# Performance work log

Measured on AMD Instinct MI355X. Metric: run time of the kernel, lower is better.

Reference implementation:

```python
import jax, jax.numpy as jnp
import numpy as np

EPS = 1e-4


def setup_inputs() -> dict:
    key = jax.random.key(0)
    k1, k2, k3, k4, k5 = jax.random.split(key, 5)
    N, M, F = 2048, 2048, 128
    embeds = jax.random.uniform(k1, (N, F), dtype=jnp.float32)
    base_embeds = jax.random.normal(k2, (M, F), dtype=jnp.float32)
    base_rewards = jax.random.normal(k3, (M,), dtype=jnp.float32)
    # torch Linear(num_feat, num_feat, bias=False) / Linear(num_feat, 1, bias=False)
    # stored here as [in, out] for x @ W convention
    W1 = jax.random.normal(k4, (F, F), dtype=jnp.float32) / np.sqrt(F)
    w2 = jax.random.normal(k5, (F, 1), dtype=jnp.float32) / np.sqrt(F)
    return {"embeds": embeds, "base_embeds": base_embeds,
            "base_rewards": base_rewards, "W1": W1, "w2": w2}


def reference(embeds, base_embeds, base_rewards, W1, w2):
    # pairwise differences: [N, M, F]
    diff = embeds[:, None, :] - base_embeds[None, :, :]
    # tiny MLP distance kernel: Linear -> ELU -> Linear, abs
    h = jax.nn.elu(jnp.einsum('nmf,fg->nmg', diff, W1))
    dist = jnp.abs(jnp.einsum('nmg,go->nmo', h, w2)[:, :, 0])  # [N, M]
    # inverse-distance normalized weights
    dist_w = 1.0 / (dist + EPS)
    dist_w = dist_w / jnp.sum(dist_w, axis=1, keepdims=True)
    rewards = jnp.sum(dist_w * base_rewards[None, :], axis=1)  # [N]
    return rewards
```

## Files before the change

kernel.cpp:

```cpp
#include <hip/hip_runtime.h>
#include <hip/hip_bf16.h>

#define F      128
#define NROWS  2048
#define MROWS  2048
#define BN     128
#define BM     64
#define MT     (MROWS/BM)
#define GC     32
#define NCH    (F/GC)
#define LDS_W  36
#define LOG2E  1.44269504088896340736f

typedef float f32x2 __attribute__((ext_vector_type(2)));
typedef float f32x4 __attribute__((ext_vector_type(4)));

__device__ __forceinline__ f32x2 lo2(f32x4 v) { return __builtin_shufflevector(v, v, 0, 1); }
__device__ __forceinline__ f32x2 hi2(f32x4 v) { return __builtin_shufflevector(v, v, 2, 3); }

__global__ __launch_bounds__(256) void proj_kernel(
    const float* __restrict__ embeds, const float* __restrict__ base,
    const float* __restrict__ W1, const float* __restrict__ w2,
    float* __restrict__ A1, float* __restrict__ AE,
    float* __restrict__ B1, float* __restrict__ BE,
    float* __restrict__ w2sum)
{
    const int tid = threadIdx.x;
    const int sub = tid >> 7;
    const int g   = tid & 127;
    const int row = blockIdx.x * 2 + sub;

    __shared__ float xs[2][F];
    {
        const float* src = (row < NROWS) ? &embeds[(size_t)row * F]
                                         : &base[(size_t)(row - NROWS) * F];
        xs[sub][g] = src[g];
    }
    __syncthreads();

    float acc = 0.0f;
#pragma unroll 8
    for (int f = 0; f < F; ++f)
        acc = fmaf(xs[sub][f], W1[f * F + g], acc);

    if (row < NROWS) {
        const size_t idx = (size_t)row * F + g;
        A1[idx] = acc + 1.0f;
        AE[idx] = __builtin_amdgcn_exp2f(acc * LOG2E);
    } else {
        const size_t idx = (size_t)(row - NROWS) * F + g;
        B1[idx] = -acc;
        BE[idx] = __builtin_amdgcn_exp2f(-acc * LOG2E);
    }

    if (blockIdx.x == 0 && tid < 64) {
        float s = w2[tid] + w2[tid + 64];
#pragma unroll
        for (int k = 1; k < 64; k <<= 1) s += __shfl_xor(s, k);
        if (tid == 0) *w2sum = s;
    }
}

__global__ __launch_bounds__(256) void pair_kernel(
    const float* __restrict__ A1, const float* __restrict__ AE,
    const float* __restrict__ B1, const float* __restrict__ BE,
    const float* __restrict__ w2, const float* __restrict__ w2sum_p,
    const float* __restrict__ brew, float* __restrict__ partials)
{
    __shared__ float As1[BN][LDS_W], AsE[BN][LDS_W];
    __shared__ float Bs1[BM][LDS_W], BsE[BM][LDS_W];
    __shared__ float w2s[F];
    __shared__ float rs[BM];

    const int tid = threadIdx.x;
    const int nt  = blockIdx.x;
    const int mt  = blockIdx.y;
    const int tr  = tid >> 4;
    const int tc  = tid & 15;

    f32x2 acc2[8][4];
#pragma unroll
    for (int i = 0; i < 8; ++i)
#pragma unroll
        for (int j = 0; j < 4; ++j) acc2[i][j] = (f32x2)(0.0f);

    if (tid < F)                 w2s[tid]     = w2[tid];
    else if (tid < F + BM)       rs[tid - F]  = brew[mt * BM + (tid - F)];

#pragma unroll 1
    for (int ch = 0; ch < NCH; ++ch) {
        const int g0 = ch * GC;
        for (int i = tid; i < 2048; i += 256) {
            const int pl = i >> 10, r = (i >> 3) & 127, c = (i & 7) * 4;
            const float* src = pl ? AE : A1;
            float* dst = pl ? &AsE[r][c] : &As1[r][c];
            *(f32x4*)dst = *(const f32x4*)&src[(size_t)(nt * BN + r) * F + g0 + c];
        }
        for (int i = tid; i < 1024; i += 256) {
            const int pl = i >> 9, r = (i >> 3) & 63, c = (i & 7) * 4;
            const float* src = pl ? BE : B1;
            float* dst = pl ? &BsE[r][c] : &Bs1[r][c];
            *(f32x4*)dst = *(const f32x4*)&src[(size_t)(mt * BM + r) * F + g0 + c];
        }
        __syncthreads();

#pragma unroll
        for (int g4 = 0; g4 < GC; g4 += 4) {
            const f32x2 w01 = *(const f32x2*)&w2s[g0 + g4];
            const f32x2 w23 = *(const f32x2*)&w2s[g0 + g4 + 2];
            f32x4 b1v[4], bev[4];
#pragma unroll
            for (int j = 0; j < 4; ++j) {
                b1v[j] = *(const f32x4*)&Bs1[tc + 16 * j][g4];
                bev[j] = *(const f32x4*)&BsE[tc + 16 * j][g4];
            }
#pragma unroll
            for (int i = 0; i < 8; ++i) {
                const f32x4 a1v = *(const f32x4*)&As1[tr + 16 * i][g4];
                const f32x4 aev = *(const f32x4*)&AsE[tr + 16 * i][g4];
                const f32x2 a1lo = lo2(a1v), a1hi = hi2(a1v);
                const f32x2 aelo = lo2(aev), aehi = hi2(aev);
#pragma unroll
                for (int j = 0; j < 4; ++j) {
                    f32x2 x1 = a1lo + lo2(b1v[j]);
                    f32x2 ee = aelo * lo2(bev[j]);
                    f32x2 s;
                    s.x = __builtin_amdgcn_fmed3f(x1.x, ee.x, 1.0f);
                    s.y = __builtin_amdgcn_fmed3f(x1.y, ee.y, 1.0f);
                    acc2[i][j] += s * w01;
                    f32x2 x2 = a1hi + hi2(b1v[j]);
                    f32x2 e2 = aehi * hi2(bev[j]);
                    f32x2 s2;
                    s2.x = __builtin_amdgcn_fmed3f(x2.x, e2.x, 1.0f);
                    s2.y = __builtin_amdgcn_fmed3f(x2.y, e2.y, 1.0f);
                    acc2[i][j] += s2 * w23;
                }
            }
        }
        __syncthreads();
    }

    const float w2sum = *w2sum_p;

#pragma unroll
    for (int i = 0; i < 8; ++i) {
        float sw = 0.0f, swr = 0.0f;
#pragma unroll
        for (int j = 0; j < 4; ++j) {
            const float tot  = acc2[i][j].x + acc2[i][j].y;
            const float dist = fabsf(tot - w2sum);
            const float w = 1.0f / (dist + 1e-4f);
            sw += w;
            swr = fmaf(w, rs[tc + 16 * j], swr);
        }
#pragma unroll
        for (int k = 1; k < 16; k <<= 1) {
            sw  += __shfl_xor(sw, k);
            swr += __shfl_xor(swr, k);
        }
        if (tc == 0) {
            const int n = nt * BN + tr + 16 * i;
            partials[((size_t)n * MT + mt) * 2 + 0] = sw;
            partials[((size_t)n * MT + mt) * 2 + 1] = swr;
        }
    }
}

__global__ __launch_bounds__(256) void finalize_kernel(
    const float* __restrict__ partials, float* __restrict__ out)
{
    const int n = blockIdx.x * 256 + threadIdx.x;
    if (n < NROWS) {
        float sw = 0.0f, swr = 0.0f;
#pragma unroll
        for (int t = 0; t < MT; ++t) {
            sw  += partials[((size_t)n * MT + t) * 2 + 0];
            swr += partials[((size_t)n * MT + t) * 2 + 1];
        }
        out[n] = swr / sw;
    }
}

extern "C" void kernel_launch(void* const* d_in, const int* in_sizes, int n_in,
                              void* d_out, int out_size, void* d_ws, size_t ws_size,
                              hipStream_t stream)
{
    const float* embeds       = (const float*)d_in[0];
    const float* base_embeds  = (const float*)d_in[1];
    const float* base_rewards = (const float*)d_in[2];
    const float* W1           = (const float*)d_in[3];
    const float* w2           = (const float*)d_in[4];
    float* out = (float*)d_out;

    float* partials = (float*)d_ws;
    float* A1  = partials + (size_t)NROWS * MT * 2;
    float* AE  = A1 + (size_t)NROWS * F;
    float* B1  = AE + (size_t)NROWS * F;
    float* BE  = B1 + (size_t)MROWS * F;
    float* w2s = BE + (size_t)MROWS * F;

    proj_kernel<<<(NROWS + MROWS) / 2, 256, 0, stream>>>(
        embeds, base_embeds, W1, w2, A1, AE, B1, BE, w2s);

    dim3 grid2(NROWS / BN, MROWS / BM);
    pair_kernel<<<grid2, 256, 0, stream>>>(A1, AE, B1, BE, w2, w2s, base_rewards, partials);

    finalize_kernel<<<(NROWS + 255) / 256, 256, 0, stream>>>(partials, out);
}
```

Measured before the change: 80.04 us.

## Fold w2 into projected operands and retile pair kernel to single-wave blocks

The projection kernel now pre-multiplies the A-side linear and exponential terms and the B-side linear term by w2. The pair kernel then evaluates w2*(ELU+1) as one med3 of (a-b, ae*be, w), removing the per-element weight multiply. The pair kernel is also restructured into 64-thread single-wavefront blocks of 64x64 tiles with an 8x8 accumulator per thread and 16-wide feature chunks. Because it is a single wave, the block barriers are dropped. In exchange it uses scalar instead of packed arithmetic, a serial accumulation chain, more blocks with less work each, and global loads of w2 inside the inner loop.

```diff
diff --git a/kernel.cpp b/kernel.cpp
--- a/kernel.cpp
+++ b/kernel.cpp
@@ -4,25 +4,21 @@
 #define F      128
 #define NROWS  2048
 #define MROWS  2048
-#define BN     128
+#define BN     64
 #define BM     64
 #define MT     (MROWS/BM)
-#define GC     32
+#define GC     16
 #define NCH    (F/GC)
-#define LDS_W  36
+#define LW     20
 #define LOG2E  1.44269504088896340736f
 
-typedef float f32x2 __attribute__((ext_vector_type(2)));
 typedef float f32x4 __attribute__((ext_vector_type(4)));
-
-__device__ __forceinline__ f32x2 lo2(f32x4 v) { return __builtin_shufflevector(v, v, 0, 1); }
-__device__ __forceinline__ f32x2 hi2(f32x4 v) { return __builtin_shufflevector(v, v, 2, 3); }
 
 __global__ __launch_bounds__(256) void proj_kernel(
     const float* __restrict__ embeds, const float* __restrict__ base,
     const float* __restrict__ W1, const float* __restrict__ w2,
-    float* __restrict__ A1, float* __restrict__ AE,
-    float* __restrict__ B1, float* __restrict__ BE,
+    float* __restrict__ A1W, float* __restrict__ AEW,
+    float* __restrict__ B1W, float* __restrict__ BEp,
     float* __restrict__ w2sum)
 {
     const int tid = threadIdx.x;
@@ -43,14 +39,15 @@
     for (int f = 0; f < F; ++f)
         acc = fmaf(xs[sub][f], W1[f * F + g], acc);
 
+    const float w = w2[g];
     if (row < NROWS) {
         const size_t idx = (size_t)row * F + g;
-        A1[idx] = acc + 1.0f;
-        AE[idx] = __builtin_amdgcn_exp2f(acc * LOG2E);
+        A1W[idx] = (acc + 1.0f) * w;
+        AEW[idx] = __builtin_amdgcn_exp2f(acc * LOG2E) * w;
     } else {
         const size_t idx = (size_t)(row - NROWS) * F + g;
-        B1[idx] = -acc;
-        BE[idx] = __builtin_amdgcn_exp2f(-acc * LOG2E);
+        B1W[idx] = acc * w;
+        BEp[idx] = __builtin_amdgcn_exp2f(-acc * LOG2E);
     }
 
     if (blockIdx.x == 0 && tid < 64) {
@@ -61,105 +58,99 @@
     }
 }
 
-__global__ __launch_bounds__(256) void pair_kernel(
-    const float* __restrict__ A1, const float* __restrict__ AE,
-    const float* __restrict__ B1, const float* __restrict__ BE,
+__global__ __launch_bounds__(64) void pair_kernel(
+    const float* __restrict__ A1W, const float* __restrict__ AEW,
+    const float* __restrict__ B1W, const float* __restrict__ BEp,
     const float* __restrict__ w2, const float* __restrict__ w2sum_p,
     const float* __restrict__ brew, float* __restrict__ partials)
 {
-    __shared__ float As1[BN][LDS_W], AsE[BN][LDS_W];
-    __shared__ float Bs1[BM][LDS_W], BsE[BM][LDS_W];
-    __shared__ float w2s[F];
-    __shared__ float rs[BM];
-
-    const int tid = threadIdx.x;
-    const int nt  = blockIdx.x;
-    const int mt  = blockIdx.y;
-    const int tr  = tid >> 4;
-    const int tc  = tid & 15;
-
-    f32x2 acc2[8][4];
+    __shared__ float sA1[BN][LW], sAE[BN][LW];
+    __shared__ float sB1[BM][LW], sBE[BM][LW];
+
+    const int lane = threadIdx.x;
+    const int nt   = blockIdx.x;
+    const int mt   = blockIdx.y;
+    const int n0   = nt * BN;
+    const int m0   = mt * BM;
+    const int tr   = lane >> 3;
+    const int tc   = lane & 7;
+
+    const float* pA1 = A1W + (size_t)n0 * F;
+    const float* pAE = AEW + (size_t)n0 * F;
+    const float* pB1 = B1W + (size_t)m0 * F;
+    const float* pBE = BEp + (size_t)m0 * F;
+
+    float acc[8][8];
 #pragma unroll
     for (int i = 0; i < 8; ++i)
 #pragma unroll
-        for (int j = 0; j < 4; ++j) acc2[i][j] = (f32x2)(0.0f);
-
-    if (tid < F)                 w2s[tid]     = w2[tid];
-    else if (tid < F + BM)       rs[tid - F]  = brew[mt * BM + (tid - F)];
+        for (int j = 0; j < 8; ++j) acc[i][j] = 0.0f;
+
+#define STAGE_PLANE(SRC, DST)                                              \
+    _Pragma("unroll")                                                      \
+    for (int rnd = 0; rnd < 4; ++rnd) {                                    \
+        const int idx = rnd * 64 + lane;                                   \
+        const int r = idx >> 2, c = (idx & 3) * 4;                         \
+        *(f32x4*)&DST[r][c] = *(const f32x4*)&SRC[(size_t)r * F + g0 + c]; \
+    }
 
 #pragma unroll 1
     for (int ch = 0; ch < NCH; ++ch) {
         const int g0 = ch * GC;
-        for (int i = tid; i < 2048; i += 256) {
-            const int pl = i >> 10, r = (i >> 3) & 127, c = (i & 7) * 4;
-            const float* src = pl ? AE : A1;
-            float* dst = pl ? &AsE[r][c] : &As1[r][c];
-            *(f32x4*)dst = *(const f32x4*)&src[(size_t)(nt * BN + r) * F + g0 + c];
-        }
-        for (int i = tid; i < 1024; i += 256) {
-            const int pl = i >> 9, r = (i >> 3) & 63, c = (i & 7) * 4;
-            const float* src = pl ? BE : B1;
-            float* dst = pl ? &BsE[r][c] : &Bs1[r][c];
-            *(f32x4*)dst = *(const f32x4*)&src[(size_t)(mt * BM + r) * F + g0 + c];
-        }
-        __syncthreads();
-
-#pragma unroll
+        STAGE_PLANE(pA1, sA1)
+        STAGE_PLANE(pAE, sAE)
+        STAGE_PLANE(pB1, sB1)
+        STAGE_PLANE(pBE, sBE)
+
+#pragma unroll 1
         for (int g4 = 0; g4 < GC; g4 += 4) {
-            const f32x2 w01 = *(const f32x2*)&w2s[g0 + g4];
-            const f32x2 w23 = *(const f32x2*)&w2s[g0 + g4 + 2];
-            f32x4 b1v[4], bev[4];
-#pragma unroll
-            for (int j = 0; j < 4; ++j) {
-                b1v[j] = *(const f32x4*)&Bs1[tc + 16 * j][g4];
-                bev[j] = *(const f32x4*)&BsE[tc + 16 * j][g4];
+            const f32x4 wv = *(const f32x4*)&w2[g0 + g4];
+            f32x4 b1v[8], bev[8];
+#pragma unroll
+            for (int j = 0; j < 8; ++j) {
+                b1v[j] = *(const f32x4*)&sB1[tc + 8 * j][g4];
+                bev[j] = *(const f32x4*)&sBE[tc + 8 * j][g4];
             }
 #pragma unroll
             for (int i = 0; i < 8; ++i) {
-                const f32x4 a1v = *(const f32x4*)&As1[tr + 16 * i][g4];
-                const f32x4 aev = *(const f32x4*)&AsE[tr + 16 * i][g4];
-                const f32x2 a1lo = lo2(a1v), a1hi = hi2(a1v);
-                const f32x2 aelo = lo2(aev), aehi = hi2(aev);
-#pragma unroll
-                for (int j = 0; j < 4; ++j) {
-                    f32x2 x1 = a1lo + lo2(b1v[j]);
-                    f32x2 ee = aelo * lo2(bev[j]);
-                    f32x2 s;
-                    s.x = __builtin_amdgcn_fmed3f(x1.x, ee.x, 1.0f);
-                    s.y = __builtin_amdgcn_fmed3f(x1.y, ee.y, 1.0f);
-                    acc2[i][j] += s * w01;
-                    f32x2 x2 = a1hi + hi2(b1v[j]);
-                    f32x2 e2 = aehi * hi2(bev[j]);
-                    f32x2 s2;
-                    s2.x = __builtin_amdgcn_fmed3f(x2.x, e2.x, 1.0f);
-                    s2.y = __builtin_amdgcn_fmed3f(x2.y, e2.y, 1.0f);
-                    acc2[i][j] += s2 * w23;
+                const f32x4 a1 = *(const f32x4*)&sA1[tr + 8 * i][g4];
+                const f32x4 ae = *(const f32x4*)&sAE[tr + 8 * i][g4];
+#pragma unroll
+                for (int j = 0; j < 8; ++j) {
+                    float d = acc[i][j];
+                    d += __builtin_amdgcn_fmed3f(a1.x - b1v[j].x, ae.x * bev[j].x, wv.x);
+                    d += __builtin_amdgcn_fmed3f(a1.y - b1v[j].y, ae.y * bev[j].y, wv.y);
+                    d += __builtin_amdgcn_fmed3f(a1.z - b1v[j].z, ae.z * bev[j].z, wv.z);
+                    d += __builtin_amdgcn_fmed3f(a1.w - b1v[j].w, ae.w * bev[j].w, wv.w);
+                    acc[i][j] = d;
                 }
             }
         }
-        __syncthreads();
-    }
+    }
+#undef STAGE_PLANE
 
     const float w2sum = *w2sum_p;
+    float rsv[8];
+#pragma unroll
+    for (int j = 0; j < 8; ++j) rsv[j] = brew[m0 + tc + 8 * j];
 
 #pragma unroll
     for (int i = 0; i < 8; ++i) {
         float sw = 0.0f, swr = 0.0f;
 #pragma unroll
-        for (int j = 0; j < 4; ++j) {
-            const float tot  = acc2[i][j].x + acc2[i][j].y;
-            const float dist = fabsf(tot - w2sum);
+        for (int j = 0; j < 8; ++j) {
+            const float dist = fabsf(acc[i][j] - w2sum);
             const float w = 1.0f / (dist + 1e-4f);
             sw += w;
-            swr = fmaf(w, rs[tc + 16 * j], swr);
-        }
-#pragma unroll
-        for (int k = 1; k < 16; k <<= 1) {
+            swr = fmaf(w, rsv[j], swr);
+        }
+#pragma unroll
+        for (int k = 1; k < 8; k <<= 1) {
             sw  += __shfl_xor(sw, k);
             swr += __shfl_xor(swr, k);
         }
         if (tc == 0) {
-            const int n = nt * BN + tr + 16 * i;
+            const int n = n0 + tr + 8 * i;
             partials[((size_t)n * MT + mt) * 2 + 0] = sw;
             partials[((size_t)n * MT + mt) * 2 + 1] = swr;
         }
@@ -193,17 +184,17 @@
     float* out = (float*)d_out;
 
     float* partials = (float*)d_ws;
-    float* A1  = partials + (size_t)NROWS * MT * 2;
-    float* AE  = A1 + (size_t)NROWS * F;
-    float* B1  = AE + (size_t)NROWS * F;
-    float* BE  = B1 + (size_t)MROWS * F;
-    float* w2s = BE + (size_t)MROWS * F;
+    float* A1W = partials + (size_t)NROWS * MT * 2;
+    float* AEW = A1W + (size_t)NROWS * F;
+    float* B1W = AEW + (size_t)NROWS * F;
+    float* BEp = B1W + (size_t)MROWS * F;
+    float* w2s = BEp + (size_t)MROWS * F;
 
     proj_kernel<<<(NROWS + MROWS) / 2, 256, 0, stream>>>(
-        embeds, base_embeds, W1, w2, A1, AE, B1, BE, w2s);
+        embeds, base_embeds, W1, w2, A1W, AEW, B1W, BEp, w2s);
 
     dim3 grid2(NROWS / BN, MROWS / BM);
-    pair_kernel<<<grid2, 256, 0, stream>>>(A1, AE, B1, BE, w2, w2s, base_rewards, partials);
+    pair_kernel<<<grid2, 64, 0, stream>>>(A1W, AEW, B1W, BEp, w2, w2s, base_rewards, partials);
 
     finalize_kernel<<<(NROWS + 255) / 256, 256, 0, stream>>>(partials, out);
 }
```

Measured after the change: 89.15 us. 1.11x slower.

## Fold w2 into projections, double-buffer tiles via global_load_lds with swizzled LDS

Applied to the files above, without the earlier changes.

The projection kernel now pre-multiplies the A-side linear and exp terms and the B-side linear term by w2, and interleaves them into one 256-float row per point grouped in 16-feature chunks. With that scaling, the median-of-three ELU evaluation uses w2 as its clamp value, so the per-pair multiply by w2 becomes a plain packed add. The pair kernel streams chunks through double-buffered LDS using direct global-to-LDS loads with an XOR swizzle, prefetching the next chunk while computing the current one. It also uses inline packed add/mul asm and sets an occupancy hint of 3 blocks. The med3 trick relies on the ordering of the scaled terms, and the asm blocks keep the compiler from rescheduling those instructions.

```diff
diff --git a/kernel.cpp b/kernel.cpp
--- a/kernel.cpp
+++ b/kernel.cpp
@@ -7,9 +7,6 @@
 #define BN     128
 #define BM     64
 #define MT     (MROWS/BM)
-#define GC     32
-#define NCH    (F/GC)
-#define LDS_W  36
 #define LOG2E  1.44269504088896340736f
 
 typedef float f32x2 __attribute__((ext_vector_type(2)));
@@ -17,12 +14,22 @@
 
 __device__ __forceinline__ f32x2 lo2(f32x4 v) { return __builtin_shufflevector(v, v, 0, 1); }
 __device__ __forceinline__ f32x2 hi2(f32x4 v) { return __builtin_shufflevector(v, v, 2, 3); }
+__device__ __forceinline__ f32x2 pk_add(f32x2 a, f32x2 b) {
+    f32x2 d; asm("v_pk_add_f32 %0, %1, %2" : "=v"(d) : "v"(a), "v"(b)); return d;
+}
+__device__ __forceinline__ f32x2 pk_mul(f32x2 a, f32x2 b) {
+    f32x2 d; asm("v_pk_mul_f32 %0, %1, %2" : "=v"(d) : "v"(a), "v"(b)); return d;
+}
+__device__ __forceinline__ void gload16(const float* g, float* l) {
+    __builtin_amdgcn_global_load_lds(
+        (const __attribute__((address_space(1))) void*)g,
+        (__attribute__((address_space(3))) void*)l, 16, 0, 0);
+}
 
 __global__ __launch_bounds__(256) void proj_kernel(
     const float* __restrict__ embeds, const float* __restrict__ base,
     const float* __restrict__ W1, const float* __restrict__ w2,
-    float* __restrict__ A1, float* __restrict__ AE,
-    float* __restrict__ B1, float* __restrict__ BE,
+    float* __restrict__ PA, float* __restrict__ PB,
     float* __restrict__ w2sum)
 {
     const int tid = threadIdx.x;
@@ -43,14 +50,16 @@
     for (int f = 0; f < F; ++f)
         acc = fmaf(xs[sub][f], W1[f * F + g], acc);
 
+    const float wv = w2[g];
+    const int   ch = g >> 4, go = g & 15;
     if (row < NROWS) {
-        const size_t idx = (size_t)row * F + g;
-        A1[idx] = acc + 1.0f;
-        AE[idx] = __builtin_amdgcn_exp2f(acc * LOG2E);
+        float* dst = PA + (size_t)row * 256 + ch * 32 + go;
+        dst[0]  = (acc + 1.0f) * wv;
+        dst[16] = __builtin_amdgcn_exp2f(acc * LOG2E) * wv;
     } else {
-        const size_t idx = (size_t)(row - NROWS) * F + g;
-        B1[idx] = -acc;
-        BE[idx] = __builtin_amdgcn_exp2f(-acc * LOG2E);
+        float* dst = PB + (size_t)(row - NROWS) * 256 + ch * 32 + go;
+        dst[0]  = -acc * wv;
+        dst[16] = __builtin_amdgcn_exp2f(-acc * LOG2E);
     }
 
     if (blockIdx.x == 0 && tid < 64) {
@@ -61,97 +70,118 @@
     }
 }
 
-__global__ __launch_bounds__(256) void pair_kernel(
-    const float* __restrict__ A1, const float* __restrict__ AE,
-    const float* __restrict__ B1, const float* __restrict__ BE,
+__global__ __launch_bounds__(256, 3) void pair_kernel(
+    const float* __restrict__ PA, const float* __restrict__ PB,
     const float* __restrict__ w2, const float* __restrict__ w2sum_p,
     const float* __restrict__ brew, float* __restrict__ partials)
 {
-    __shared__ float As1[BN][LDS_W], AsE[BN][LDS_W];
-    __shared__ float Bs1[BM][LDS_W], BsE[BM][LDS_W];
-    __shared__ float w2s[F];
-    __shared__ float rs[BM];
+    __shared__ float sbuf[2][6144];
+    __shared__ float w2l[F];
 
     const int tid = threadIdx.x;
-    const int nt  = blockIdx.x;
-    const int mt  = blockIdx.y;
-    const int tr  = tid >> 4;
-    const int tc  = tid & 15;
-
-    f32x2 acc2[8][4];
+    const int w    = tid >> 6;
+    const int l    = tid & 63;
+    const int nt   = blockIdx.x, mt = blockIdx.y;
+    const int n0   = nt * BN,    m0 = mt * BM;
+    const int tr   = tid >> 4,   tc = tid & 15;
+    const int fa   = (tr & 7) * 4,  fb = (tc & 7) * 4;
+    const int rsub = l >> 3;
+    const int lswz = 4 * ((l & 7) ^ rsub);
+
+#define STAGE(CH, BUF) {                                                        \
+    const float* pa = PA + (size_t)(n0 + rsub) * 256 + (CH) * 32 + lswz;        \
+    _Pragma("unroll")                                                           \
+    for (int t = 0; t < 4; ++t) {                                               \
+        const int k = t * 4 + w;                                                \
+        gload16(pa + (size_t)(8 * k) * 256, &sbuf[BUF][k * 256]);               \
+    }                                                                           \
+    const float* pb = PB + (size_t)(m0 + rsub) * 256 + (CH) * 32 + lswz;        \
+    _Pragma("unroll")                                                           \
+    for (int t = 0; t < 2; ++t) {                                               \
+        const int k = t * 4 + w;                                                \
+        gload16(pb + (size_t)(8 * k) * 256, &sbuf[BUF][4096 + k * 256]);        \
+    } }
+
+    f32x2 acc2[8][2];
 #pragma unroll
     for (int i = 0; i < 8; ++i)
 #pragma unroll
-        for (int j = 0; j < 4; ++j) acc2[i][j] = (f32x2)(0.0f);
-
-    if (tid < F)                 w2s[tid]     = w2[tid];
-    else if (tid < F + BM)       rs[tid - F]  = brew[mt * BM + (tid - F)];
+        for (int jj = 0; jj < 2; ++jj) acc2[i][jj] = (f32x2)(0.0f);
+
+    STAGE(0, 0)
+    if (tid < F) w2l[tid] = w2[tid];
+    __syncthreads();
 
 #pragma unroll 1
-    for (int ch = 0; ch < NCH; ++ch) {
-        const int g0 = ch * GC;
-        for (int i = tid; i < 2048; i += 256) {
-            const int pl = i >> 10, r = (i >> 3) & 127, c = (i & 7) * 4;
-            const float* src = pl ? AE : A1;
-            float* dst = pl ? &AsE[r][c] : &As1[r][c];
-            *(f32x4*)dst = *(const f32x4*)&src[(size_t)(nt * BN + r) * F + g0 + c];
-        }
-        for (int i = tid; i < 1024; i += 256) {
-            const int pl = i >> 9, r = (i >> 3) & 63, c = (i & 7) * 4;
-            const float* src = pl ? BE : B1;
-            float* dst = pl ? &BsE[r][c] : &Bs1[r][c];
-            *(f32x4*)dst = *(const f32x4*)&src[(size_t)(mt * BM + r) * F + g0 + c];
-        }
-        __syncthreads();
-
-#pragma unroll
-        for (int g4 = 0; g4 < GC; g4 += 4) {
-            const f32x2 w01 = *(const f32x2*)&w2s[g0 + g4];
-            const f32x2 w23 = *(const f32x2*)&w2s[g0 + g4 + 2];
+    for (int ch = 0; ch < 8; ++ch) {
+        const int buf = ch & 1;
+        if (ch < 7) STAGE(ch + 1, buf ^ 1);
+
+        const float* sb = sbuf[buf];
+#pragma unroll
+        for (int g4 = 0; g4 < 16; g4 += 4) {
+            const f32x4 wq = *(const f32x4*)&w2l[ch * 16 + g4];
             f32x4 b1v[4], bev[4];
 #pragma unroll
             for (int j = 0; j < 4; ++j) {
-                b1v[j] = *(const f32x4*)&Bs1[tc + 16 * j][g4];
-                bev[j] = *(const f32x4*)&BsE[tc + 16 * j][g4];
+                const float* bb = sb + 4096 + (tc + 16 * j) * 32;
+                b1v[j] = *(const f32x4*)&bb[g4 ^ fb];
+                bev[j] = *(const f32x4*)&bb[(16 + g4) ^ fb];
             }
 #pragma unroll
             for (int i = 0; i < 8; ++i) {
-                const f32x4 a1v = *(const f32x4*)&As1[tr + 16 * i][g4];
-                const f32x4 aev = *(const f32x4*)&AsE[tr + 16 * i][g4];
-                const f32x2 a1lo = lo2(a1v), a1hi = hi2(a1v);
-                const f32x2 aelo = lo2(aev), aehi = hi2(aev);
-#pragma unroll
-                for (int j = 0; j < 4; ++j) {
-                    f32x2 x1 = a1lo + lo2(b1v[j]);
-                    f32x2 ee = aelo * lo2(bev[j]);
-                    f32x2 s;
-                    s.x = __builtin_amdgcn_fmed3f(x1.x, ee.x, 1.0f);
-                    s.y = __builtin_amdgcn_fmed3f(x1.y, ee.y, 1.0f);
-                    acc2[i][j] += s * w01;
-                    f32x2 x2 = a1hi + hi2(b1v[j]);
-                    f32x2 e2 = aehi * hi2(bev[j]);
-                    f32x2 s2;
-                    s2.x = __builtin_amdgcn_fmed3f(x2.x, e2.x, 1.0f);
-                    s2.y = __builtin_amdgcn_fmed3f(x2.y, e2.y, 1.0f);
-                    acc2[i][j] += s2 * w23;
+                const float* ab = sb + (tr + 16 * i) * 32;
+                const f32x4 a1 = *(const f32x4*)&ab[g4 ^ fa];
+                const f32x4 ae = *(const f32x4*)&ab[(16 + g4) ^ fa];
+                const f32x2 a1l = lo2(a1), a1h = hi2(a1);
+                const f32x2 ael = lo2(ae), aeh = hi2(ae);
+#pragma unroll
+                for (int jj = 0; jj < 2; ++jj) {
+                    const f32x2 xl0 = pk_add(a1l, lo2(b1v[2 * jj]));
+                    const f32x2 xh0 = pk_add(a1h, hi2(b1v[2 * jj]));
+                    const f32x2 el0 = pk_mul(ael, lo2(bev[2 * jj]));
+                    const f32x2 eh0 = pk_mul(aeh, hi2(bev[2 * jj]));
+                    const f32x2 xl1 = pk_add(a1l, lo2(b1v[2 * jj + 1]));
+                    const f32x2 xh1 = pk_add(a1h, hi2(b1v[2 * jj + 1]));
+                    const f32x2 el1 = pk_mul(ael, lo2(bev[2 * jj + 1]));
+                    const f32x2 eh1 = pk_mul(aeh, hi2(bev[2 * jj + 1]));
+                    f32x2 s0, s1, s2, s3;
+                    s0.x = __builtin_amdgcn_fmed3f(xl0.x, el0.x, wq.x);
+                    s0.y = __builtin_amdgcn_fmed3f(xl1.x, el1.x, wq.x);
+                    s1.x = __builtin_amdgcn_fmed3f(xl0.y, el0.y, wq.y);
+                    s1.y = __builtin_amdgcn_fmed3f(xl1.y, el1.y, wq.y);
+                    s2.x = __builtin_amdgcn_fmed3f(xh0.x, eh0.x, wq.z);
+                    s2.y = __builtin_amdgcn_fmed3f(xh1.x, eh1.x, wq.z);
+                    s3.x = __builtin_amdgcn_fmed3f(xh0.y, eh0.y, wq.w);
+                    s3.y = __builtin_amdgcn_fmed3f(xh1.y, eh1.y, wq.w);
+                    f32x2 t = acc2[i][jj];
+                    t = pk_add(t, s0);
+                    t = pk_add(t, s1);
+                    t = pk_add(t, s2);
+                    t = pk_add(t, s3);
+                    acc2[i][jj] = t;
                 }
             }
         }
         __syncthreads();
     }
+#undef STAGE
 
     const float w2sum = *w2sum_p;
+    float rsv[4];
+#pragma unroll
+    for (int j = 0; j < 4; ++j) rsv[j] = brew[m0 + tc + 16 * j];
 
 #pragma unroll
     for (int i = 0; i < 8; ++i) {
         float sw = 0.0f, swr = 0.0f;
 #pragma unroll
         for (int j = 0; j < 4; ++j) {
-            const float tot  = acc2[i][j].x + acc2[i][j].y;
+            const float tot  = (j & 1) ? acc2[i][j >> 1].y : acc2[i][j >> 1].x;
             const float dist = fabsf(tot - w2sum);
-            const float w = 1.0f / (dist + 1e-4f);
-            sw += w;
-            swr = fmaf(w, rs[tc + 16 * j], swr);
+            const float wgt  = 1.0f / (dist + 1e-4f);
+            sw += wgt;
+            swr = fmaf(wgt, rsv[j], swr);
         }
 #pragma unroll
         for (int k = 1; k < 16; k <<= 1) {
@@ -159,7 +189,7 @@
             swr += __shfl_xor(swr, k);
         }
         if (tc == 0) {
-            const int n = nt * BN + tr + 16 * i;
+            const int n = n0 + tr + 16 * i;
             partials[((size_t)n * MT + mt) * 2 + 0] = sw;
             partials[((size_t)n * MT + mt) * 2 + 1] = swr;
         }
@@ -193,17 +223,15 @@
     float* out = (float*)d_out;
 
     float* partials = (float*)d_ws;
-    float* A1  = partials + (size_t)NROWS * MT * 2;
-    float* AE  = A1 + (size_t)NROWS * F;
-    float* B1  = AE + (size_t)NROWS * F;
-    float* BE  = B1 + (size_t)MROWS * F;
-    float* w2s = BE + (size_t)MROWS * F;
+    float* PA  = partials + (size_t)NROWS * MT * 2;
+    float* PB  = PA + (size_t)NROWS * 256;
+    float* w2s = PB + (size_t)MROWS * 256;
 
     proj_kernel<<<(NROWS + MROWS) / 2, 256, 0, stream>>>(
-        embeds, base_embeds, W1, w2, A1, AE, B1, BE, w2s);
+        embeds, base_embeds, W1, w2, PA, PB, w2s);
 
     dim3 grid2(NROWS / BN, MROWS / BM);
-    pair_kernel<<<grid2, 256, 0, stream>>>(A1, AE, B1, BE, w2, w2s, base_rewards, partials);
+    pair_kernel<<<grid2, 256, 0, stream>>>(PA, PB, w2, w2s, base_rewards, partials);
 
     finalize_kernel<<<(NROWS + 255) / 256, 256, 0, stream>>>(partials, out);
 }
```

New measurement: 74.94 us. -6.4%, faster.
